# Kernel tuning notes

Hardware: AMD Instinct MI355X
Metric: run time of the kernel (lower is better)

The kernel has to match this reference:

```python
import jax, jax.numpy as jnp
import numpy as np

B, T, C = 4, 2048, 1024
H = 16
HD = C // H  # 64


def setup_inputs() -> dict:
    key = jax.random.key(0)
    k1, k2, k3 = jax.random.split(key, 3)
    x = jax.random.normal(k1, (B, T, C), dtype=jnp.float32)
    W_attn = jax.random.normal(k2, (C, 3 * C), dtype=jnp.float32) * (1.0 / np.sqrt(C))
    b_attn = jnp.zeros((3 * C,), dtype=jnp.float32)
    W_proj = jax.random.normal(k3, (C, C), dtype=jnp.float32) * (1.0 / np.sqrt(C))
    b_proj = jnp.zeros((C,), dtype=jnp.float32)
    return {"x": x, "W_attn": W_attn, "b_attn": b_attn, "W_proj": W_proj, "b_proj": b_proj}


def reference(x, W_attn, b_attn, W_proj, b_proj):
    Bx, Tx, Cx = x.shape
    qkv = x @ W_attn + b_attn                      # [B,T,3C]
    q, k, v = jnp.split(qkv, 3, axis=-1)
    # [B,T,C] -> [B,H,T,HD]
    q = q.reshape(Bx, Tx, H, HD).transpose(0, 2, 1, 3)
    k = k.reshape(Bx, Tx, H, HD).transpose(0, 2, 1, 3)
    v = v.reshape(Bx, Tx, H, HD).transpose(0, 2, 1, 3)
    att = jnp.einsum('bhqd,bhkd->bhqk', q, k) / jnp.sqrt(jnp.float32(HD))
    causal = jnp.tril(jnp.ones((Tx, Tx), dtype=bool))
    att = jnp.where(causal[None, None], att, -jnp.inf)
    att = jax.nn.softmax(att, axis=-1)
    y = jnp.einsum('bhqk,bhkd->bhqd', att, v)      # [B,H,T,HD]
    y = y.transpose(0, 2, 1, 3).reshape(Bx, Tx, Cx)
    return y @ W_proj + b_proj
```

## Files before the change

### kernel.cpp

```cpp
#include <hip/hip_runtime.h>
#include <hip/hip_bf16.h>

typedef unsigned short u16;
typedef __attribute__((ext_vector_type(8))) short bf16x8;
typedef __attribute__((ext_vector_type(4))) float f32x4;

#define MFMA16(a, b, c) __builtin_amdgcn_mfma_f32_16x16x32_bf16((a), (b), (c), 0, 0, 0)

__device__ __forceinline__ u16 f2bf(float f) {
  union { float f; unsigned u; } v; v.f = f;
  unsigned r = v.u + 0x7fffu + ((v.u >> 16) & 1u);
  return (u16)(r >> 16);
}

__device__ __forceinline__ unsigned pk_trunc(float hi, float lo) {
  union { float f; unsigned u; } a, b; a.f = hi; b.f = lo;
  return __builtin_amdgcn_perm(a.u, b.u, 0x07060302u);
}

__device__ __forceinline__ void gload_lds16(const u16* g, u16* l) {
  __builtin_amdgcn_global_load_lds((const __attribute__((address_space(1))) void*)g,
                                   (__attribute__((address_space(3))) void*)l, 16, 0, 0);
}

__global__ __launch_bounds__(256) void convert_bf16_k(const float* __restrict__ in,
                                                      u16* __restrict__ out, int n) {
  int i = (blockIdx.x * 256 + threadIdx.x) * 8;
  if (i >= n) return;
  float4 v0 = *(const float4*)(in + i);
  float4 v1 = *(const float4*)(in + i + 4);
  uint4 o;
  o.x = (unsigned)f2bf(v0.x) | ((unsigned)f2bf(v0.y) << 16);
  o.y = (unsigned)f2bf(v0.z) | ((unsigned)f2bf(v0.w) << 16);
  o.z = (unsigned)f2bf(v1.x) | ((unsigned)f2bf(v1.y) << 16);
  o.w = (unsigned)f2bf(v1.z) | ((unsigned)f2bf(v1.w) << 16);
  *(uint4*)(out + i) = o;
}

__global__ __launch_bounds__(256) void transpose2_k(const float* __restrict__ Wa, u16* __restrict__ WaT,
                                                    const float* __restrict__ Wp, u16* __restrict__ WpT) {
  __shared__ float tile[64][65];
  int b = blockIdx.x;
  const float* W; u16* Wt; int N, n0, k0;
  if (b < 768) { W = Wa; Wt = WaT; N = 3072; n0 = (b % 48) * 64; k0 = (b / 48) * 64; }
  else { int c = b - 768; W = Wp; Wt = WpT; N = 1024; n0 = (c & 15) * 64; k0 = (c >> 4) * 64; }
  const int tx = threadIdx.x & 63, ty = threadIdx.x >> 6;
#pragma unroll
  for (int i = 0; i < 16; ++i)
    tile[ty + 4 * i][tx] = W[(size_t)(k0 + ty + 4 * i) * N + n0 + tx];
  __syncthreads();
#pragma unroll
  for (int i = 0; i < 16; ++i)
    Wt[(size_t)(n0 + ty + 4 * i) * 1024 + k0 + tx] = f2bf(tile[tx][ty + 4 * i]);
}

#define GEMM_PROLOG                                                                \
  __shared__ u16 As[128 * 32];                                                     \
  __shared__ u16 Bs[128 * 32];                                                     \
  const int tid = threadIdx.x;                                                     \
  const int w = tid >> 6, lane = tid & 63;                                         \
  const int wm = w & 1, wn = w >> 1;                                               \
  const int fr = lane & 15, fg = lane >> 4;                                        \
  const int srow = lane >> 2, skof = (lane & 3) * 8;                               \
  u16* lA = As + w * 1024;                                                         \
  u16* lB = Bs + w * 1024;                                                         \
  f32x4 acc[4][4];                                                                 \
  _Pragma("unroll") for (int i = 0; i < 4; i++)                                    \
      _Pragma("unroll") for (int j = 0; j < 4; j++) acc[i][j] = (f32x4){0, 0, 0, 0};

#define GEMM_KLOOP(Aptr, Btptr, SWAP)                                              \
  {                                                                                \
    const u16* gA0 = (Aptr) + (size_t)(m0 + w * 32 + srow) * 1024 + skof;          \
    const u16* gB0 = (Btptr) + (size_t)(n0 + w * 32 + srow) * 1024 + skof;         \
    for (int kt = 0; kt < 32; ++kt) {                                              \
      const int ko = kt * 32;                                                      \
      gload_lds16(gA0 + ko, lA);                                                   \
      gload_lds16(gA0 + ko + 16 * 1024, lA + 512);                                 \
      gload_lds16(gB0 + ko, lB);                                                   \
      gload_lds16(gB0 + ko + 16 * 1024, lB + 512);                                 \
      __syncthreads();                                                             \
      bf16x8 af[4], bfr[4];                                                        \
      _Pragma("unroll") for (int mb = 0; mb < 4; ++mb)                             \
          af[mb] = *(const bf16x8*)&As[(wm * 64 + mb * 16 + fr) * 32 + fg * 8];    \
      _Pragma("unroll") for (int nb = 0; nb < 4; ++nb)                             \
          bfr[nb] = *(const bf16x8*)&Bs[(wn * 64 + nb * 16 + fr) * 32 + fg * 8];   \
      _Pragma("unroll") for (int mb = 0; mb < 4; ++mb)                             \
          _Pragma("unroll") for (int nb = 0; nb < 4; ++nb)                         \
              acc[mb][nb] = (SWAP) ? MFMA16(bfr[nb], af[mb], acc[mb][nb])          \
                                   : MFMA16(af[mb], bfr[nb], acc[mb][nb]);         \
      __syncthreads();                                                             \
    }                                                                              \
  }

__global__ __launch_bounds__(256) void gemm_qkv(const u16* __restrict__ A,
                                                const u16* __restrict__ Bt,
                                                const float* __restrict__ bias,
                                                u16* __restrict__ Qo, u16* __restrict__ Ko,
                                                u16* __restrict__ Vt) {
  const int m0 = blockIdx.y * 128, n0 = blockIdx.x * 128;
  GEMM_PROLOG
  GEMM_KLOOP(A, Bt, 0)
  const int which = n0 >> 10;
#pragma unroll
  for (int nb = 0; nb < 4; ++nb) {
    const int n = n0 + wn * 64 + nb * 16 + fr;
    const float bs = bias[n];
    const int c = n & 1023, h = c >> 6, hd = c & 63;
#pragma unroll
    for (int mb = 0; mb < 4; ++mb) {
      const int mbase = m0 + wm * 64 + mb * 16 + fg * 4;
      const int bb = mbase >> 11;
      const int t = mbase & 2047;
      if (which == 0) {
        u16* dst = Qo + ((size_t)(bb * 16 + h) * 2048 + t) * 64 + hd;
#pragma unroll
        for (int r = 0; r < 4; ++r) dst[(size_t)r * 64] = f2bf((acc[mb][nb][r] + bs) * 0.125f);
      } else if (which == 1) {
        u16* dst = Ko + ((size_t)(bb * 16 + h) * 2048 + t) * 64 + hd;
#pragma unroll
        for (int r = 0; r < 4; ++r) dst[(size_t)r * 64] = f2bf(acc[mb][nb][r] + bs);
      } else {
        ushort4 pv;
        pv.x = f2bf(acc[mb][nb][0] + bs);
        pv.y = f2bf(acc[mb][nb][1] + bs);
        pv.z = f2bf(acc[mb][nb][2] + bs);
        pv.w = f2bf(acc[mb][nb][3] + bs);
        *(ushort4*)(Vt + ((size_t)(bb * 16 + h) * 64 + hd) * 2048 + t) = pv;
      }
    }
  }
}

__global__ __launch_bounds__(256) void gemm_proj(const u16* __restrict__ A,
                                                 const u16* __restrict__ Bt,
                                                 const float* __restrict__ bias,
                                                 float* __restrict__ O) {
  const int id = blockIdx.x;
  const int m0 = (id >> 3) * 128, n0 = (id & 7) * 128;
  GEMM_PROLOG
  GEMM_KLOOP(A, Bt, 1)
#pragma unroll
  for (int mb = 0; mb < 4; ++mb) {
    const int tg = m0 + wm * 64 + mb * 16 + fr;
#pragma unroll
    for (int nb = 0; nb < 4; ++nb) {
      const int n = n0 + wn * 64 + nb * 16 + 4 * fg;
      const float4 b4 = *(const float4*)(bias + n);
      float4 o;
      o.x = acc[mb][nb][0] + b4.x;
      o.y = acc[mb][nb][1] + b4.y;
      o.z = acc[mb][nb][2] + b4.z;
      o.w = acc[mb][nb][3] + b4.w;
      *(float4*)(O + (size_t)tg * 1024 + n) = o;
    }
  }
}

#define PSTR 72
__global__ __launch_bounds__(256) void attn_k(const u16* __restrict__ Q,
                                              const u16* __restrict__ Kb,
                                              const u16* __restrict__ Vt,
                                              u16* __restrict__ Y) {
  __shared__ u16 Ks[64 * 72];
  __shared__ u16 Vs[64 * 72];
  __shared__ u16 Ps[4 * 32 * PSTR];
  const int L = blockIdx.x;
  const int xcd = L & 7, slot = L >> 3;
  const int bh = xcd * 8 + (slot & 7);
  const int qt = 15 - (slot >> 3);
  const int tid = threadIdx.x, w = tid >> 6, lane = tid & 63;
  const int fr = lane & 15, fg = lane >> 4;
  const u16* Qp = Q + (size_t)bh * 2048 * 64;
  const u16* Kp = Kb + (size_t)bh * 2048 * 64;
  const u16* Vp = Vt + (size_t)bh * 64 * 2048;
  const int qw = qt * 128 + w * 32;

  bf16x8 qa[2][2];
#pragma unroll
  for (int g = 0; g < 2; ++g)
#pragma unroll
    for (int c = 0; c < 2; ++c)
      qa[g][c] = *(const bf16x8*)(Qp + (size_t)(qw + g * 16 + fr) * 64 + c * 32 + fg * 8);

  float li[2] = {0.f, 0.f};
  f32x4 ot[2][4];
#pragma unroll
  for (int g = 0; g < 2; ++g)
#pragma unroll
    for (int mb = 0; mb < 4; ++mb) ot[g][mb] = (f32x4){0, 0, 0, 0};

  const int srow = tid >> 2, scol = (tid & 3) * 16;
  u16* Pw = Ps + w * 32 * PSTR;
  const int nk = 2 * qt + 2;
  const u16* Kg = Kp + (size_t)srow * 64 + scol;
  const u16* Vg = Vp + (size_t)srow * 2048 + scol;

  uint4 kr0 = *(const uint4*)(Kg);
  uint4 kr1 = *(const uint4*)(Kg + 8);
  uint4 vr0 = *(const uint4*)(Vg);
  uint4 vr1 = *(const uint4*)(Vg + 8);

  for (int jt = 0; jt < nk; ++jt) {
    const int k0 = jt * 64;
    if (jt) __syncthreads();
    *(uint4*)&Ks[srow * 72 + scol] = kr0;
    *(uint4*)&Ks[srow * 72 + scol + 8] = kr1;
    *(uint4*)&Vs[srow * 72 + scol] = vr0;
    *(uint4*)&Vs[srow * 72 + scol + 8] = vr1;
    __syncthreads();
    if (jt + 1 < nk) {
      const int kn = (jt + 1) * 64;
      kr0 = *(const uint4*)(Kg + (size_t)kn * 64);
      kr1 = *(const uint4*)(Kg + (size_t)kn * 64 + 8);
      vr0 = *(const uint4*)(Vg + kn);
      vr1 = *(const uint4*)(Vg + kn + 8);
    }
    if (k0 > qw + 31) continue;

    bf16x8 kb[4][2];
#pragma unroll
    for (int nb = 0; nb < 4; ++nb) {
      kb[nb][0] = *(const bf16x8*)&Ks[(nb * 16 + fr) * 72 + fg * 8];
      kb[nb][1] = *(const bf16x8*)&Ks[(nb * 16 + fr) * 72 + 32 + fg * 8];
    }
    f32x4 st[2][4];
#pragma unroll
    for (int g = 0; g < 2; ++g)
#pragma unroll
      for (int nb = 0; nb < 4; ++nb) {
        f32x4 z = (f32x4){0, 0, 0, 0};
        z = MFMA16(kb[nb][0], qa[g][0], z);
        z = MFMA16(kb[nb][1], qa[g][1], z);
        st[g][nb] = z;
      }
    const bool needmask = (k0 + 63 > qw);
#pragma unroll
    for (int g = 0; g < 2; ++g) {
      const int q = qw + g * 16 + fr;
      float rs0 = 0.f, rs1 = 0.f;
#pragma unroll
      for (int nb = 0; nb < 4; ++nb) {
        const int kcb = k0 + nb * 16 + 4 * fg;
        float p0 = __expf(st[g][nb][0]);
        float p1 = __expf(st[g][nb][1]);
        float p2 = __expf(st[g][nb][2]);
        float p3 = __expf(st[g][nb][3]);
        if (needmask) {
          p0 = (kcb + 0 > q) ? 0.f : p0;
          p1 = (kcb + 1 > q) ? 0.f : p1;
          p2 = (kcb + 2 > q) ? 0.f : p2;
          p3 = (kcb + 3 > q) ? 0.f : p3;
        }
        rs0 += p0 + p1;
        rs1 += p2 + p3;
        *(uint2*)&Pw[(g * 16 + fr) * PSTR + nb * 16 + 4 * fg] =
            make_uint2(pk_trunc(p1, p0), pk_trunc(p3, p2));
      }
      li[g] += rs0 + rs1;
    }
    bf16x8 pa[2][2];
#pragma unroll
    for (int g = 0; g < 2; ++g)
#pragma unroll
      for (int H = 0; H < 2; ++H)
        pa[g][H] = *(const bf16x8*)&Pw[(g * 16 + fr) * PSTR + H * 32 + fg * 8];
#pragma unroll
    for (int mb = 0; mb < 4; ++mb) {
      bf16x8 vb0 = *(const bf16x8*)&Vs[(mb * 16 + fr) * 72 + fg * 8];
      bf16x8 vb1 = *(const bf16x8*)&Vs[(mb * 16 + fr) * 72 + 32 + fg * 8];
#pragma unroll
      for (int g = 0; g < 2; ++g) {
        ot[g][mb] = MFMA16(vb0, pa[g][0], ot[g][mb]);
        ot[g][mb] = MFMA16(vb1, pa[g][1], ot[g][mb]);
      }
    }
  }

  const int b = bh >> 4, h = bh & 15;
#pragma unroll
  for (int g = 0; g < 2; ++g) {
    float l = li[g];
    l += __shfl_xor(l, 16);
    l += __shfl_xor(l, 32);
    const float inv = 1.0f / l;
    const int t = qw + g * 16 + fr;
    u16* yrow = Y + ((size_t)b * 2048 + t) * 1024 + h * 64;
#pragma unroll
    for (int mb = 0; mb < 4; ++mb) {
      const unsigned d0 = (unsigned)f2bf(ot[g][mb][0] * inv) |
                          ((unsigned)f2bf(ot[g][mb][1] * inv) << 16);
      const unsigned d1 = (unsigned)f2bf(ot[g][mb][2] * inv) |
                          ((unsigned)f2bf(ot[g][mb][3] * inv) << 16);
      *(uint2*)&yrow[mb * 16 + fg * 4] = make_uint2(d0, d1);
    }
  }
}

extern "C" void kernel_launch(void* const* d_in, const int* in_sizes, int n_in,
                              void* d_out, int out_size, void* d_ws, size_t ws_size,
                              hipStream_t stream) {
  const float* x = (const float*)d_in[0];
  const float* Wa = (const float*)d_in[1];
  const float* ba = (const float*)d_in[2];
  const float* Wp = (const float*)d_in[3];
  const float* bp = (const float*)d_in[4];
  float* out = (float*)d_out;

  char* p = (char*)d_ws;
  u16* xb = (u16*)p;   p += (size_t)8192 * 1024 * 2;
  u16* WaT = (u16*)p;  p += (size_t)3072 * 1024 * 2;
  u16* WpT = (u16*)p;  p += (size_t)1024 * 1024 * 2;
  u16* Qb = (u16*)p;   p += (size_t)64 * 2048 * 64 * 2;
  u16* Kbuf = (u16*)p; p += (size_t)64 * 2048 * 64 * 2;
  u16* Vtb = (u16*)p;  p += (size_t)64 * 64 * 2048 * 2;
  u16* Yb = (u16*)p;   p += (size_t)8192 * 1024 * 2;

  convert_bf16_k<<<4096, 256, 0, stream>>>(x, xb, 8192 * 1024);
  transpose2_k<<<1024, 256, 0, stream>>>(Wa, WaT, Wp, WpT);
  gemm_qkv<<<dim3(24, 64), 256, 0, stream>>>(xb, WaT, ba, Qb, Kbuf, Vtb);
  attn_k<<<1024, 256, 0, stream>>>(Qb, Kbuf, Vtb, Yb);
  gemm_proj<<<512, 256, 0, stream>>>(Yb, WpT, bp, out);
}
```

Measured before the change: 269.3 us.

## Rewrite QKV GEMM as 256x256 tile, 8-wave, double-buffered pipelined kernel

Replaces the 128x128 single-buffered QKV GEMM with a 256x256-tile kernel of 512 threads. Each block double-buffers K=64 slices in LDS and interleaves global-to-LDS loads for the next stage between four MFMA phases, using explicit barriers, waitcnt and setprio. It also swizzles the LDS layout and remaps block indices for L2 locality. The goal is to hide global load latency and raise MFMA utilization, at the cost of more LDS and register use and fragile hand-written synchronization.

```diff
diff --git a/kernel.cpp b/kernel.cpp
--- a/kernel.cpp
+++ b/kernel.cpp
@@ -92,14 +92,92 @@
     }                                                                              \
   }
 
-__global__ __launch_bounds__(256) void gemm_qkv(const u16* __restrict__ A,
-                                                const u16* __restrict__ Bt,
-                                                const float* __restrict__ bias,
-                                                u16* __restrict__ Qo, u16* __restrict__ Ko,
-                                                u16* __restrict__ Vt) {
-  const int m0 = blockIdx.y * 128, n0 = blockIdx.x * 128;
-  GEMM_PROLOG
-  GEMM_KLOOP(A, Bt, 0)
+#define BAR() asm volatile("s_barrier" ::: "memory")
+#define WLG()                                                   \
+  do {                                                          \
+    asm volatile("s_waitcnt lgkmcnt(0)" ::: "memory");          \
+    __builtin_amdgcn_sched_barrier(0);                          \
+  } while (0)
+
+__global__ __launch_bounds__(512, 2) void gemm_qkv_8p(const u16* __restrict__ A,
+                                                      const u16* __restrict__ Bt,
+                                                      const float* __restrict__ bias,
+                                                      u16* __restrict__ Qo, u16* __restrict__ Ko,
+                                                      u16* __restrict__ Vt) {
+  __shared__ u16 sm[2][2][16384];
+  const int bid = blockIdx.x;
+  const int swz = (bid & 7) * 48 + (bid >> 3);
+  const int m0 = (swz / 12) * 256, n0 = (swz % 12) * 256;
+  const int tid = threadIdx.x, w = tid >> 6, lane = tid & 63;
+  const int wm = w >> 2, wn = w & 3;
+  const int fr = lane & 15, fg = lane >> 4;
+
+  const int sr = lane >> 2;
+  const int sk = (lane & 1) * 8 + ((((lane >> 1) ^ (lane >> 5)) & 1) << 4);
+  const int kc = (w & 1) * 32 + sk;
+  const int r0 = (w >> 1) * 16 + sr;
+  const int lsw = fr * 32 + ((fg * 8) ^ ((fr & 8) ? 16 : 0));
+
+  const u16* gA00 = A + (size_t)(m0 + r0) * 1024 + kc;
+  const u16* gB00 = Bt + (size_t)(n0 + r0) * 1024 + kc;
+
+#define STG_(mat, base, tt, h, c)                                                    \
+  gload_lds16((base) + (size_t)(h) * 131072 + (c) * 65536 + (size_t)(tt) * 64,       \
+              &sm[(tt) & 1][mat][(h) * 8192 + (c) * 4096 + w * 512])
+
+  f32x4 acc[8][4];
+#pragma unroll
+  for (int i = 0; i < 8; ++i)
+#pragma unroll
+    for (int j = 0; j < 4; ++j) acc[i][j] = (f32x4){0, 0, 0, 0};
+
+  STG_(0, gA00, 0, 0, 0); STG_(0, gA00, 0, 0, 1);
+  STG_(0, gA00, 0, 1, 0); STG_(0, gA00, 0, 1, 1);
+  STG_(1, gB00, 0, 0, 0); STG_(1, gB00, 0, 0, 1);
+  STG_(1, gB00, 0, 1, 0); STG_(1, gB00, 0, 1, 1);
+  STG_(1, gB00, 1, 0, 0); STG_(1, gB00, 1, 0, 1);
+  asm volatile("s_waitcnt vmcnt(2)" ::: "memory");
+  BAR();
+
+#define LDA4(KK, MB0)                                                     \
+  _Pragma("unroll") for (int i = 0; i < 4; ++i)                           \
+      av[i] = *(const bf16x8*)(ard + ((MB0 + i) * 2 + (KK)) * 512);
+#define LDB4(KK)                                                          \
+  _Pragma("unroll") for (int i = 0; i < 4; ++i)                           \
+      bv[i] = *(const bf16x8*)(brd + (i * 2 + (KK)) * 512);
+#define MM16(MB0)                                                         \
+  __builtin_amdgcn_s_setprio(1);                                          \
+  _Pragma("unroll") for (int i = 0; i < 4; ++i)                           \
+      _Pragma("unroll") for (int j = 0; j < 4; ++j)                       \
+          acc[MB0 + i][j] = MFMA16(av[i], bv[j], acc[MB0 + i][j]);        \
+  __builtin_amdgcn_s_setprio(0);
+
+  for (int t = 0; t < 16; ++t) {
+    const int b = t & 1;
+    const u16* ard = &sm[b][0][wm * 8192 + lsw];
+    const u16* brd = &sm[b][1][(wn >> 1) * 8192 + (wn & 1) * 4096 + lsw];
+    bf16x8 av[4], bv[4];
+
+    LDA4(0, 0); LDB4(0);
+    if (t + 1 < 16) { STG_(1, gB00, t + 1, 1, 0); STG_(1, gB00, t + 1, 1, 1); }
+    BAR(); WLG(); MM16(0); BAR();
+
+    LDA4(0, 4);
+    if (t + 1 < 16) { STG_(0, gA00, t + 1, 0, 0); STG_(0, gA00, t + 1, 0, 1); }
+    BAR(); WLG(); MM16(4); BAR();
+
+    LDA4(1, 0); LDB4(1);
+    if (t + 1 < 16) { STG_(0, gA00, t + 1, 1, 0); STG_(0, gA00, t + 1, 1, 1); }
+    BAR(); WLG(); MM16(0); BAR();
+
+    LDA4(1, 4);
+    if (t + 2 < 16) { STG_(1, gB00, t + 2, 0, 0); STG_(1, gB00, t + 2, 0, 1); }
+    BAR(); WLG(); MM16(4);
+    if (t + 2 < 16)      asm volatile("s_waitcnt vmcnt(2)" ::: "memory");
+    else if (t + 1 < 16) asm volatile("s_waitcnt vmcnt(0)" ::: "memory");
+    BAR();
+  }
+
   const int which = n0 >> 10;
 #pragma unroll
   for (int nb = 0; nb < 4; ++nb) {
@@ -107,16 +185,16 @@
     const float bs = bias[n];
     const int c = n & 1023, h = c >> 6, hd = c & 63;
 #pragma unroll
-    for (int mb = 0; mb < 4; ++mb) {
-      const int mbase = m0 + wm * 64 + mb * 16 + fg * 4;
+    for (int mb = 0; mb < 8; ++mb) {
+      const int mbase = m0 + wm * 128 + mb * 16 + fg * 4;
       const int bb = mbase >> 11;
-      const int t = mbase & 2047;
+      const int tt = mbase & 2047;
       if (which == 0) {
-        u16* dst = Qo + ((size_t)(bb * 16 + h) * 2048 + t) * 64 + hd;
+        u16* dst = Qo + ((size_t)(bb * 16 + h) * 2048 + tt) * 64 + hd;
 #pragma unroll
         for (int r = 0; r < 4; ++r) dst[(size_t)r * 64] = f2bf((acc[mb][nb][r] + bs) * 0.125f);
       } else if (which == 1) {
-        u16* dst = Ko + ((size_t)(bb * 16 + h) * 2048 + t) * 64 + hd;
+        u16* dst = Ko + ((size_t)(bb * 16 + h) * 2048 + tt) * 64 + hd;
 #pragma unroll
         for (int r = 0; r < 4; ++r) dst[(size_t)r * 64] = f2bf(acc[mb][nb][r] + bs);
       } else {
@@ -125,7 +203,7 @@
         pv.y = f2bf(acc[mb][nb][1] + bs);
         pv.z = f2bf(acc[mb][nb][2] + bs);
         pv.w = f2bf(acc[mb][nb][3] + bs);
-        *(ushort4*)(Vt + ((size_t)(bb * 16 + h) * 64 + hd) * 2048 + t) = pv;
+        *(ushort4*)(Vt + ((size_t)(bb * 16 + h) * 64 + hd) * 2048 + tt) = pv;
       }
     }
   }
@@ -317,7 +395,7 @@
 
   convert_bf16_k<<<4096, 256, 0, stream>>>(x, xb, 8192 * 1024);
   transpose2_k<<<1024, 256, 0, stream>>>(Wa, WaT, Wp, WpT);
-  gemm_qkv<<<dim3(24, 64), 256, 0, stream>>>(xb, WaT, ba, Qb, Kbuf, Vtb);
+  gemm_qkv_8p<<<384, 512, 0, stream>>>(xb, WaT, ba, Qb, Kbuf, Vtb);
   attn_k<<<1024, 256, 0, stream>>>(Qb, Kbuf, Vtb, Yb);
   gemm_proj<<<512, 256, 0, stream>>>(Yb, WpT, bp, out);
 }
```

Result: faster. 262.6 us (-2.5%).

## Rewrite QKV and projection GEMMs as double-buffered 8-wave 256-tile kernels

Applied to the files above, without the earlier changes.

Both GEMMs move from 128x128 tiles with 4 waves and a single LDS buffer to 512-thread blocks with 256-wide tiles (256x256 for QKV, 256x128 for proj) and a K-step of 64. Each step prefetches the next tile into a second LDS buffer while MFMAs run on the current one. The kernels also add XOR-swizzled LDS addressing, XCD-aware block swizzling, s_setprio around the MFMA bursts, and explicit waitcnt/barrier scheduling. The aim is to hide global-load latency and raise data reuse per block, at the cost of more LDS and registers per block and a proj epilogue that now uses scalar strided stores.

```diff
diff --git a/kernel.cpp b/kernel.cpp
--- a/kernel.cpp
+++ b/kernel.cpp
@@ -54,52 +54,97 @@
     Wt[(size_t)(n0 + ty + 4 * i) * 1024 + k0 + tx] = f2bf(tile[tx][ty + 4 * i]);
 }
 
-#define GEMM_PROLOG                                                                \
-  __shared__ u16 As[128 * 32];                                                     \
-  __shared__ u16 Bs[128 * 32];                                                     \
-  const int tid = threadIdx.x;                                                     \
-  const int w = tid >> 6, lane = tid & 63;                                         \
-  const int wm = w & 1, wn = w >> 1;                                               \
-  const int fr = lane & 15, fg = lane >> 4;                                        \
-  const int srow = lane >> 2, skof = (lane & 3) * 8;                               \
-  u16* lA = As + w * 1024;                                                         \
-  u16* lB = Bs + w * 1024;                                                         \
-  f32x4 acc[4][4];                                                                 \
-  _Pragma("unroll") for (int i = 0; i < 4; i++)                                    \
-      _Pragma("unroll") for (int j = 0; j < 4; j++) acc[i][j] = (f32x4){0, 0, 0, 0};
-
-#define GEMM_KLOOP(Aptr, Btptr, SWAP)                                              \
-  {                                                                                \
-    const u16* gA0 = (Aptr) + (size_t)(m0 + w * 32 + srow) * 1024 + skof;          \
-    const u16* gB0 = (Btptr) + (size_t)(n0 + w * 32 + srow) * 1024 + skof;         \
-    for (int kt = 0; kt < 32; ++kt) {                                              \
-      const int ko = kt * 32;                                                      \
-      gload_lds16(gA0 + ko, lA);                                                   \
-      gload_lds16(gA0 + ko + 16 * 1024, lA + 512);                                 \
-      gload_lds16(gB0 + ko, lB);                                                   \
-      gload_lds16(gB0 + ko + 16 * 1024, lB + 512);                                 \
-      __syncthreads();                                                             \
-      bf16x8 af[4], bfr[4];                                                        \
-      _Pragma("unroll") for (int mb = 0; mb < 4; ++mb)                             \
-          af[mb] = *(const bf16x8*)&As[(wm * 64 + mb * 16 + fr) * 32 + fg * 8];    \
-      _Pragma("unroll") for (int nb = 0; nb < 4; ++nb)                             \
-          bfr[nb] = *(const bf16x8*)&Bs[(wn * 64 + nb * 16 + fr) * 32 + fg * 8];   \
-      _Pragma("unroll") for (int mb = 0; mb < 4; ++mb)                             \
-          _Pragma("unroll") for (int nb = 0; nb < 4; ++nb)                         \
-              acc[mb][nb] = (SWAP) ? MFMA16(bfr[nb], af[mb], acc[mb][nb])          \
-                                   : MFMA16(af[mb], bfr[nb], acc[mb][nb]);         \
-      __syncthreads();                                                             \
-    }                                                                              \
-  }
-
-__global__ __launch_bounds__(256) void gemm_qkv(const u16* __restrict__ A,
-                                                const u16* __restrict__ Bt,
-                                                const float* __restrict__ bias,
-                                                u16* __restrict__ Qo, u16* __restrict__ Ko,
-                                                u16* __restrict__ Vt) {
-  const int m0 = blockIdx.y * 128, n0 = blockIdx.x * 128;
-  GEMM_PROLOG
-  GEMM_KLOOP(A, Bt, 0)
+#define BAR() asm volatile("s_barrier" ::: "memory")
+#define WLG()                                                   \
+  do {                                                          \
+    asm volatile("s_waitcnt lgkmcnt(0)" ::: "memory");          \
+    __builtin_amdgcn_sched_barrier(0);                          \
+  } while (0)
+#define VMW0() asm volatile("s_waitcnt vmcnt(0)" ::: "memory")
+
+#define LANE_CONSTS                                                       \
+  const int tid = threadIdx.x, w = tid >> 6, lane = tid & 63;             \
+  const int wm = w >> 2, wn = w & 3;                                      \
+  const int fr = lane & 15, fg = lane >> 4;                               \
+  const int sr = lane >> 2;                                               \
+  const int sk = (lane & 1) * 8 + ((((lane >> 1) ^ (lane >> 5)) & 1) << 4); \
+  const int kc = (w & 1) * 32 + sk;                                       \
+  const int r0g = (w >> 1) * 16 + sr;                                     \
+  const int lsw = fr * 32 + ((fg * 8) ^ ((fr & 8) ? 16 : 0));
+
+__global__ __launch_bounds__(512, 2) void gemm_qkv_8p(const u16* __restrict__ A,
+                                                      const u16* __restrict__ Bt,
+                                                      const float* __restrict__ bias,
+                                                      u16* __restrict__ Qo, u16* __restrict__ Ko,
+                                                      u16* __restrict__ Vt) {
+  __shared__ u16 sm[2][32768];
+  const int bid = blockIdx.x;
+  const int swz = (bid & 7) * 48 + (bid >> 3);
+  const int m0 = (swz / 12) * 256, n0 = (swz % 12) * 256;
+  LANE_CONSTS
+  const int aoff = wm * 8192 + lsw;
+  const int boff = 16384 + (wn >> 1) * 8192 + (wn & 1) * 4096 + lsw;
+
+  const u16* gA = A + (size_t)(m0 + r0g) * 1024 + kc;
+  const u16* gB = Bt + (size_t)(n0 + r0g) * 1024 + kc;
+
+#define QSTGA(D, H, C) \
+  gload_lds16(gA + (size_t)(H) * 131072 + (C) * 65536, &sm[(D)][(H) * 8192 + (C) * 4096 + w * 512])
+#define QSTGB(D, H, C) \
+  gload_lds16(gB + (size_t)(H) * 131072 + (C) * 65536, &sm[(D)][16384 + (H) * 8192 + (C) * 4096 + w * 512])
+
+  f32x4 acc[8][4];
+#pragma unroll
+  for (int i = 0; i < 8; ++i)
+#pragma unroll
+    for (int j = 0; j < 4; ++j) acc[i][j] = (f32x4){0, 0, 0, 0};
+
+  QSTGA(0, 0, 0); QSTGA(0, 0, 1); QSTGA(0, 1, 0); QSTGA(0, 1, 1);
+  QSTGB(0, 0, 0); QSTGB(0, 0, 1); QSTGB(0, 1, 0); QSTGB(0, 1, 1);
+  gA += 64; gB += 64;
+  VMW0(); BAR();
+
+#define QLDA(B_, KK, M0_)                                                 \
+  _Pragma("unroll") for (int i = 0; i < 4; ++i)                           \
+      av[i] = *(const bf16x8*)&sm[(B_)][aoff + (((M0_) + i) * 2 + (KK)) * 512];
+#define QLDB(B_, KK)                                                      \
+  _Pragma("unroll") for (int i = 0; i < 4; ++i)                           \
+      bv[i] = *(const bf16x8*)&sm[(B_)][boff + (i * 2 + (KK)) * 512];
+#define QMM(MB0)                                                          \
+  __builtin_amdgcn_s_setprio(1);                                          \
+  _Pragma("unroll") for (int i = 0; i < 4; ++i)                           \
+      _Pragma("unroll") for (int j = 0; j < 4; ++j)                       \
+          acc[(MB0) + i][j] = MFMA16(av[i], bv[j], acc[(MB0) + i][j]);    \
+  __builtin_amdgcn_s_setprio(0);
+
+#define QTILE(B_, S_)                                                          \
+  {                                                                            \
+    bf16x8 av[4], bv[4];                                                       \
+                       \
+    QLDA(B_, 0, 0) QLDB(B_, 0)                                                 \
+    if (S_) { QSTGA((B_) ^ 1, 0, 0); QSTGA((B_) ^ 1, 0, 1);                    \
+              QSTGA((B_) ^ 1, 1, 0); QSTGA((B_) ^ 1, 1, 1); }                  \
+    BAR(); WLG(); QMM(0) BAR();                                                \
+                               \
+    QLDA(B_, 0, 4)                                                             \
+    if (S_) { QSTGB((B_) ^ 1, 0, 0); QSTGB((B_) ^ 1, 0, 1);                    \
+              QSTGB((B_) ^ 1, 1, 0); QSTGB((B_) ^ 1, 1, 1); }                  \
+    BAR(); WLG(); QMM(4) BAR();                                                \
+                                                  \
+    QLDA(B_, 1, 0) QLDB(B_, 1)                                                 \
+    BAR(); WLG(); QMM(0) BAR();                                                \
+                       \
+    QLDA(B_, 1, 4)                                                             \
+    BAR(); WLG(); QMM(4)                                                       \
+    if (S_) { VMW0(); gA += 64; gB += 64; }                                    \
+    BAR();                                                                     \
+  }
+
+#pragma unroll 1
+  for (int tp = 0; tp < 7; ++tp) { QTILE(0, 1) QTILE(1, 1) }
+  QTILE(0, 1)
+  QTILE(1, 0)
+
   const int which = n0 >> 10;
 #pragma unroll
   for (int nb = 0; nb < 4; ++nb) {
@@ -107,16 +152,16 @@
     const float bs = bias[n];
     const int c = n & 1023, h = c >> 6, hd = c & 63;
 #pragma unroll
-    for (int mb = 0; mb < 4; ++mb) {
-      const int mbase = m0 + wm * 64 + mb * 16 + fg * 4;
+    for (int mb = 0; mb < 8; ++mb) {
+      const int mbase = m0 + wm * 128 + mb * 16 + fg * 4;
       const int bb = mbase >> 11;
-      const int t = mbase & 2047;
+      const int tt = mbase & 2047;
       if (which == 0) {
-        u16* dst = Qo + ((size_t)(bb * 16 + h) * 2048 + t) * 64 + hd;
+        u16* dst = Qo + ((size_t)(bb * 16 + h) * 2048 + tt) * 64 + hd;
 #pragma unroll
         for (int r = 0; r < 4; ++r) dst[(size_t)r * 64] = f2bf((acc[mb][nb][r] + bs) * 0.125f);
       } else if (which == 1) {
-        u16* dst = Ko + ((size_t)(bb * 16 + h) * 2048 + t) * 64 + hd;
+        u16* dst = Ko + ((size_t)(bb * 16 + h) * 2048 + tt) * 64 + hd;
 #pragma unroll
         for (int r = 0; r < 4; ++r) dst[(size_t)r * 64] = f2bf(acc[mb][nb][r] + bs);
       } else {
@@ -125,35 +170,102 @@
         pv.y = f2bf(acc[mb][nb][1] + bs);
         pv.z = f2bf(acc[mb][nb][2] + bs);
         pv.w = f2bf(acc[mb][nb][3] + bs);
-        *(ushort4*)(Vt + ((size_t)(bb * 16 + h) * 64 + hd) * 2048 + t) = pv;
+        *(ushort4*)(Vt + ((size_t)(bb * 16 + h) * 64 + hd) * 2048 + tt) = pv;
       }
     }
   }
-}
-
-__global__ __launch_bounds__(256) void gemm_proj(const u16* __restrict__ A,
-                                                 const u16* __restrict__ Bt,
-                                                 const float* __restrict__ bias,
-                                                 float* __restrict__ O) {
-  const int id = blockIdx.x;
-  const int m0 = (id >> 3) * 128, n0 = (id & 7) * 128;
-  GEMM_PROLOG
-  GEMM_KLOOP(A, Bt, 1)
-#pragma unroll
-  for (int mb = 0; mb < 4; ++mb) {
-    const int tg = m0 + wm * 64 + mb * 16 + fr;
-#pragma unroll
-    for (int nb = 0; nb < 4; ++nb) {
-      const int n = n0 + wn * 64 + nb * 16 + 4 * fg;
-      const float4 b4 = *(const float4*)(bias + n);
-      float4 o;
-      o.x = acc[mb][nb][0] + b4.x;
-      o.y = acc[mb][nb][1] + b4.y;
-      o.z = acc[mb][nb][2] + b4.z;
-      o.w = acc[mb][nb][3] + b4.w;
-      *(float4*)(O + (size_t)tg * 1024 + n) = o;
-    }
-  }
+#undef QSTGA
+#undef QSTGB
+#undef QLDA
+#undef QLDB
+#undef QMM
+#undef QTILE
+}
+
+__global__ __launch_bounds__(512, 2) void gemm_proj_8p(const u16* __restrict__ A,
+                                                       const u16* __restrict__ Bt,
+                                                       const float* __restrict__ bias,
+                                                       float* __restrict__ O) {
+  __shared__ u16 sm[2][24576];
+  const int bid = blockIdx.x;
+  const int swz = (bid & 7) * 32 + (bid >> 3);
+  const int m0 = (swz >> 3) * 256, n0 = (swz & 7) * 128;
+  LANE_CONSTS
+  const int aoff = wm * 8192 + lsw;
+  const int boff = 16384 + wn * 2048 + lsw;
+
+  const u16* gA = A + (size_t)(m0 + r0g) * 1024 + kc;
+  const u16* gB = Bt + (size_t)(n0 + r0g) * 1024 + kc;
+
+#define PSTGA(D, H, C) \
+  gload_lds16(gA + (size_t)(H) * 131072 + (C) * 65536, &sm[(D)][(H) * 8192 + (C) * 4096 + w * 512])
+#define PSTGB(D, C) \
+  gload_lds16(gB + (size_t)(C) * 65536, &sm[(D)][16384 + (C) * 4096 + w * 512])
+
+  f32x4 acc[8][2];
+#pragma unroll
+  for (int i = 0; i < 8; ++i)
+#pragma unroll
+    for (int j = 0; j < 2; ++j) acc[i][j] = (f32x4){0, 0, 0, 0};
+
+  PSTGA(0, 0, 0); PSTGA(0, 0, 1); PSTGA(0, 1, 0); PSTGA(0, 1, 1);
+  PSTGB(0, 0); PSTGB(0, 1);
+  gA += 64; gB += 64;
+  VMW0(); BAR();
+
+#define PLDA(B_, KK, M0_)                                                 \
+  _Pragma("unroll") for (int i = 0; i < 4; ++i)                           \
+      av[i] = *(const bf16x8*)&sm[(B_)][aoff + (((M0_) + i) * 2 + (KK)) * 512];
+#define PLDB(B_, KK)                                                      \
+  _Pragma("unroll") for (int i = 0; i < 2; ++i)                           \
+      bv[i] = *(const bf16x8*)&sm[(B_)][boff + (i * 2 + (KK)) * 512];
+#define PMM(MB0)                                                          \
+  __builtin_amdgcn_s_setprio(1);                                          \
+  _Pragma("unroll") for (int i = 0; i < 4; ++i)                           \
+      _Pragma("unroll") for (int j = 0; j < 2; ++j)                       \
+          acc[(MB0) + i][j] = MFMA16(av[i], bv[j], acc[(MB0) + i][j]);    \
+  __builtin_amdgcn_s_setprio(0);
+
+#define PTILE(B_, S_)                                                          \
+  {                                                                            \
+    bf16x8 av[4], bv[2];                                                       \
+    PLDA(B_, 0, 0) PLDB(B_, 0)                                                 \
+    if (S_) { PSTGA((B_) ^ 1, 0, 0); PSTGA((B_) ^ 1, 0, 1);                    \
+              PSTGA((B_) ^ 1, 1, 0); PSTGA((B_) ^ 1, 1, 1); }                  \
+    BAR(); WLG(); PMM(0) BAR();                                                \
+    PLDA(B_, 0, 4)                                                             \
+    if (S_) { PSTGB((B_) ^ 1, 0); PSTGB((B_) ^ 1, 1); }                        \
+    BAR(); WLG(); PMM(4) BAR();                                                \
+    PLDA(B_, 1, 0) PLDB(B_, 1)                                                 \
+    BAR(); WLG(); PMM(0) BAR();                                                \
+    PLDA(B_, 1, 4)                                                             \
+    BAR(); WLG(); PMM(4)                                                       \
+    if (S_) { VMW0(); gA += 64; gB += 64; }                                    \
+    BAR();                                                                     \
+  }
+
+#pragma unroll 1
+  for (int tp = 0; tp < 7; ++tp) { PTILE(0, 1) PTILE(1, 1) }
+  PTILE(0, 1)
+  PTILE(1, 0)
+
+#pragma unroll
+  for (int nb = 0; nb < 2; ++nb) {
+    const int n = n0 + wn * 32 + nb * 16 + fr;
+    const float bs = bias[n];
+#pragma unroll
+    for (int mb = 0; mb < 8; ++mb) {
+      const int tg = m0 + wm * 128 + mb * 16 + fg * 4;
+#pragma unroll
+      for (int r = 0; r < 4; ++r) O[(size_t)(tg + r) * 1024 + n] = acc[mb][nb][r] + bs;
+    }
+  }
+#undef PSTGA
+#undef PSTGB
+#undef PLDA
+#undef PLDB
+#undef PMM
+#undef PTILE
 }
 
 #define PSTR 72
@@ -317,7 +429,7 @@
 
   convert_bf16_k<<<4096, 256, 0, stream>>>(x, xb, 8192 * 1024);
   transpose2_k<<<1024, 256, 0, stream>>>(Wa, WaT, Wp, WpT);
-  gemm_qkv<<<dim3(24, 64), 256, 0, stream>>>(xb, WaT, ba, Qb, Kbuf, Vtb);
+  gemm_qkv_8p<<<384, 512, 0, stream>>>(xb, WaT, ba, Qb, Kbuf, Vtb);
   attn_k<<<1024, 256, 0, stream>>>(Qb, Kbuf, Vtb, Yb);
-  gemm_proj<<<512, 256, 0, stream>>>(Yb, WpT, bp, out);
-}
+  gemm_proj_8p<<<256, 512, 0, stream>>>(Yb, WpT, bp, out);
+}
```

After: 254.3 us. -5.6%, faster.

## Double-buffer GEMM K-loop with swizzled LDS, larger QKV tiles, XCD-aware block mapping

Applied to the files above, without the earlier changes.

Both projection GEMMs are rewritten to double-buffer LDS so the next K-slice's global-to-LDS loads are issued before the current slice's MFMAs, which halves the barriers per K step. LDS columns are XOR-swizzled to reduce bank conflicts. The QKV GEMM moves to 128x256 tiles with each wave owning a 128x64 slab, and block IDs are remapped so consecutive blocks land on the same XCD for L2 reuse. The projection GEMM's epilogue now writes scalars in a different pattern, and the larger accumulator tiles raise register pressure.

```diff
diff --git a/kernel.cpp b/kernel.cpp
--- a/kernel.cpp
+++ b/kernel.cpp
@@ -54,69 +54,89 @@
     Wt[(size_t)(n0 + ty + 4 * i) * 1024 + k0 + tx] = f2bf(tile[tx][ty + 4 * i]);
 }
 
-#define GEMM_PROLOG                                                                \
-  __shared__ u16 As[128 * 32];                                                     \
-  __shared__ u16 Bs[128 * 32];                                                     \
-  const int tid = threadIdx.x;                                                     \
-  const int w = tid >> 6, lane = tid & 63;                                         \
-  const int wm = w & 1, wn = w >> 1;                                               \
-  const int fr = lane & 15, fg = lane >> 4;                                        \
-  const int srow = lane >> 2, skof = (lane & 3) * 8;                               \
-  u16* lA = As + w * 1024;                                                         \
-  u16* lB = Bs + w * 1024;                                                         \
-  f32x4 acc[4][4];                                                                 \
-  _Pragma("unroll") for (int i = 0; i < 4; i++)                                    \
-      _Pragma("unroll") for (int j = 0; j < 4; j++) acc[i][j] = (f32x4){0, 0, 0, 0};
-
-#define GEMM_KLOOP(Aptr, Btptr, SWAP)                                              \
-  {                                                                                \
-    const u16* gA0 = (Aptr) + (size_t)(m0 + w * 32 + srow) * 1024 + skof;          \
-    const u16* gB0 = (Btptr) + (size_t)(n0 + w * 32 + srow) * 1024 + skof;         \
-    for (int kt = 0; kt < 32; ++kt) {                                              \
-      const int ko = kt * 32;                                                      \
-      gload_lds16(gA0 + ko, lA);                                                   \
-      gload_lds16(gA0 + ko + 16 * 1024, lA + 512);                                 \
-      gload_lds16(gB0 + ko, lB);                                                   \
-      gload_lds16(gB0 + ko + 16 * 1024, lB + 512);                                 \
-      __syncthreads();                                                             \
-      bf16x8 af[4], bfr[4];                                                        \
-      _Pragma("unroll") for (int mb = 0; mb < 4; ++mb)                             \
-          af[mb] = *(const bf16x8*)&As[(wm * 64 + mb * 16 + fr) * 32 + fg * 8];    \
-      _Pragma("unroll") for (int nb = 0; nb < 4; ++nb)                             \
-          bfr[nb] = *(const bf16x8*)&Bs[(wn * 64 + nb * 16 + fr) * 32 + fg * 8];   \
-      _Pragma("unroll") for (int mb = 0; mb < 4; ++mb)                             \
-          _Pragma("unroll") for (int nb = 0; nb < 4; ++nb)                         \
-              acc[mb][nb] = (SWAP) ? MFMA16(bfr[nb], af[mb], acc[mb][nb])          \
-                                   : MFMA16(af[mb], bfr[nb], acc[mb][nb]);         \
-      __syncthreads();                                                             \
-    }                                                                              \
-  }
-
-__global__ __launch_bounds__(256) void gemm_qkv(const u16* __restrict__ A,
-                                                const u16* __restrict__ Bt,
-                                                const float* __restrict__ bias,
-                                                u16* __restrict__ Qo, u16* __restrict__ Ko,
-                                                u16* __restrict__ Vt) {
-  const int m0 = blockIdx.y * 128, n0 = blockIdx.x * 128;
-  GEMM_PROLOG
-  GEMM_KLOOP(A, Bt, 0)
+
+#define GEMM_LANE_CONSTS                                                    \
+  const int tid = threadIdx.x, w = tid >> 6, lane = tid & 63;               \
+  const int fr = lane & 15, fg = lane >> 4;                                 \
+  const int swS = ((fr >> 1) & 3) << 3;                                     \
+  const int srow = tid >> 2;                                                \
+  const int scol = ((tid & 3) * 8) ^ (((tid >> 3) & 3) << 3);
+
+__global__ __launch_bounds__(256, 2) void gemm_qkv_v2(const u16* __restrict__ A,
+                                                      const u16* __restrict__ Bt,
+                                                      const float* __restrict__ bias,
+                                                      u16* __restrict__ Qo, u16* __restrict__ Ko,
+                                                      u16* __restrict__ Vt) {
+  __shared__ u16 sm[2][12288];
+  const int bid = blockIdx.x;
+  const int swz = (bid & 7) * 96 + (bid >> 3);
+  const int m0 = (swz / 12) * 128, n0 = (swz % 12) * 256;
+  GEMM_LANE_CONSTS
+
+  const u16* gA = A + (size_t)(m0 + srow) * 1024 + scol;
+  const u16* gB = Bt + (size_t)(n0 + srow) * 1024 + scol;
+
+#define VSTGA(D, C) gload_lds16(gA + (size_t)(C) * 65536, &sm[(D)][(C) * 2048 + tid * 8])
+#define VSTGB(D, C) gload_lds16(gB + (size_t)(C) * 65536, &sm[(D)][4096 + (C) * 2048 + tid * 8])
+
+  f32x4 acc[8][4];
+#pragma unroll
+  for (int i = 0; i < 8; ++i)
+#pragma unroll
+    for (int j = 0; j < 4; ++j) acc[i][j] = (f32x4){0, 0, 0, 0};
+
+  VSTGA(0, 0); VSTGA(0, 1);
+  VSTGB(0, 0); VSTGB(0, 1); VSTGB(0, 2); VSTGB(0, 3);
+  gA += 32; gB += 32;
+  __syncthreads();
+
+  const int aoff = fr * 32 + ((fg * 8) ^ swS);
+  const int boff = 4096 + w * 2048 + fr * 32 + ((fg * 8) ^ swS);
+
+#define VTILE(B_, S_)                                                          \
+  {                                                                            \
+    if (S_) { VSTGA((B_) ^ 1, 0); VSTGA((B_) ^ 1, 1);                          \
+              VSTGB((B_) ^ 1, 0); VSTGB((B_) ^ 1, 1);                          \
+              VSTGB((B_) ^ 1, 2); VSTGB((B_) ^ 1, 3); }                        \
+    bf16x8 av[4], bv[4];                                                       \
+    _Pragma("unroll") for (int nb = 0; nb < 4; ++nb)                           \
+        bv[nb] = *(const bf16x8*)&sm[(B_)][boff + nb * 512];                   \
+    _Pragma("unroll") for (int i = 0; i < 4; ++i)                              \
+        av[i] = *(const bf16x8*)&sm[(B_)][aoff + i * 512];                     \
+    _Pragma("unroll") for (int i = 0; i < 4; ++i)                              \
+        _Pragma("unroll") for (int nb = 0; nb < 4; ++nb)                       \
+            acc[i][nb] = MFMA16(av[i], bv[nb], acc[i][nb]);                    \
+    _Pragma("unroll") for (int i = 0; i < 4; ++i)                              \
+        av[i] = *(const bf16x8*)&sm[(B_)][aoff + (4 + i) * 512];               \
+    _Pragma("unroll") for (int i = 0; i < 4; ++i)                              \
+        _Pragma("unroll") for (int nb = 0; nb < 4; ++nb)                       \
+            acc[4 + i][nb] = MFMA16(av[i], bv[nb], acc[4 + i][nb]);            \
+    if (S_) { gA += 32; gB += 32; }                                            \
+    __syncthreads();                                                           \
+  }
+
+#pragma unroll 1
+  for (int tp = 0; tp < 15; ++tp) { VTILE(0, 1) VTILE(1, 1) }
+  VTILE(0, 1)
+  VTILE(1, 0)
+
   const int which = n0 >> 10;
 #pragma unroll
   for (int nb = 0; nb < 4; ++nb) {
-    const int n = n0 + wn * 64 + nb * 16 + fr;
+    const int n = n0 + w * 64 + nb * 16 + fr;
     const float bs = bias[n];
     const int c = n & 1023, h = c >> 6, hd = c & 63;
 #pragma unroll
-    for (int mb = 0; mb < 4; ++mb) {
-      const int mbase = m0 + wm * 64 + mb * 16 + fg * 4;
+    for (int mb = 0; mb < 8; ++mb) {
+      const int mbase = m0 + mb * 16 + fg * 4;
       const int bb = mbase >> 11;
-      const int t = mbase & 2047;
+      const int tt = mbase & 2047;
       if (which == 0) {
-        u16* dst = Qo + ((size_t)(bb * 16 + h) * 2048 + t) * 64 + hd;
+        u16* dst = Qo + ((size_t)(bb * 16 + h) * 2048 + tt) * 64 + hd;
 #pragma unroll
         for (int r = 0; r < 4; ++r) dst[(size_t)r * 64] = f2bf((acc[mb][nb][r] + bs) * 0.125f);
       } else if (which == 1) {
-        u16* dst = Ko + ((size_t)(bb * 16 + h) * 2048 + t) * 64 + hd;
+        u16* dst = Ko + ((size_t)(bb * 16 + h) * 2048 + tt) * 64 + hd;
 #pragma unroll
         for (int r = 0; r < 4; ++r) dst[(size_t)r * 64] = f2bf(acc[mb][nb][r] + bs);
       } else {
@@ -125,35 +145,85 @@
         pv.y = f2bf(acc[mb][nb][1] + bs);
         pv.z = f2bf(acc[mb][nb][2] + bs);
         pv.w = f2bf(acc[mb][nb][3] + bs);
-        *(ushort4*)(Vt + ((size_t)(bb * 16 + h) * 64 + hd) * 2048 + t) = pv;
+        *(ushort4*)(Vt + ((size_t)(bb * 16 + h) * 64 + hd) * 2048 + tt) = pv;
       }
     }
   }
-}
-
-__global__ __launch_bounds__(256) void gemm_proj(const u16* __restrict__ A,
-                                                 const u16* __restrict__ Bt,
-                                                 const float* __restrict__ bias,
-                                                 float* __restrict__ O) {
-  const int id = blockIdx.x;
-  const int m0 = (id >> 3) * 128, n0 = (id & 7) * 128;
-  GEMM_PROLOG
-  GEMM_KLOOP(A, Bt, 1)
-#pragma unroll
-  for (int mb = 0; mb < 4; ++mb) {
-    const int tg = m0 + wm * 64 + mb * 16 + fr;
-#pragma unroll
-    for (int nb = 0; nb < 4; ++nb) {
-      const int n = n0 + wn * 64 + nb * 16 + 4 * fg;
-      const float4 b4 = *(const float4*)(bias + n);
-      float4 o;
-      o.x = acc[mb][nb][0] + b4.x;
-      o.y = acc[mb][nb][1] + b4.y;
-      o.z = acc[mb][nb][2] + b4.z;
-      o.w = acc[mb][nb][3] + b4.w;
-      *(float4*)(O + (size_t)tg * 1024 + n) = o;
-    }
-  }
+#undef VSTGA
+#undef VSTGB
+#undef VTILE
+}
+
+__global__ __launch_bounds__(256, 4) void gemm_proj_v2(const u16* __restrict__ A,
+                                                       const u16* __restrict__ Bt,
+                                                       const float* __restrict__ bias,
+                                                       float* __restrict__ O) {
+  __shared__ u16 sm[2][8192];
+  const int bid = blockIdx.x;
+  const int swz = (bid & 7) * 64 + (bid >> 3);
+  const int m0 = (swz >> 3) * 128, n0 = (swz & 7) * 128;
+  GEMM_LANE_CONSTS
+
+  const u16* gA = A + (size_t)(m0 + srow) * 1024 + scol;
+  const u16* gB = Bt + (size_t)(n0 + srow) * 1024 + scol;
+
+#define PSTGA(D, C) gload_lds16(gA + (size_t)(C) * 65536, &sm[(D)][(C) * 2048 + tid * 8])
+#define PSTGB(D, C) gload_lds16(gB + (size_t)(C) * 65536, &sm[(D)][4096 + (C) * 2048 + tid * 8])
+
+  f32x4 acc[8][2];
+#pragma unroll
+  for (int i = 0; i < 8; ++i)
+#pragma unroll
+    for (int j = 0; j < 2; ++j) acc[i][j] = (f32x4){0, 0, 0, 0};
+
+  PSTGA(0, 0); PSTGA(0, 1);
+  PSTGB(0, 0); PSTGB(0, 1);
+  gA += 32; gB += 32;
+  __syncthreads();
+
+  const int aoff = fr * 32 + ((fg * 8) ^ swS);
+  const int boff = 4096 + w * 1024 + fr * 32 + ((fg * 8) ^ swS);
+
+#define PTILE(B_, S_)                                                          \
+  {                                                                            \
+    if (S_) { PSTGA((B_) ^ 1, 0); PSTGA((B_) ^ 1, 1);                          \
+              PSTGB((B_) ^ 1, 0); PSTGB((B_) ^ 1, 1); }                        \
+    bf16x8 av[4], bv[2];                                                       \
+    _Pragma("unroll") for (int nb = 0; nb < 2; ++nb)                           \
+        bv[nb] = *(const bf16x8*)&sm[(B_)][boff + nb * 512];                   \
+    _Pragma("unroll") for (int i = 0; i < 4; ++i)                              \
+        av[i] = *(const bf16x8*)&sm[(B_)][aoff + i * 512];                     \
+    _Pragma("unroll") for (int i = 0; i < 4; ++i)                              \
+        _Pragma("unroll") for (int nb = 0; nb < 2; ++nb)                       \
+            acc[i][nb] = MFMA16(av[i], bv[nb], acc[i][nb]);                    \
+    _Pragma("unroll") for (int i = 0; i < 4; ++i)                              \
+        av[i] = *(const bf16x8*)&sm[(B_)][aoff + (4 + i) * 512];               \
+    _Pragma("unroll") for (int i = 0; i < 4; ++i)                              \
+        _Pragma("unroll") for (int nb = 0; nb < 2; ++nb)                       \
+            acc[4 + i][nb] = MFMA16(av[i], bv[nb], acc[4 + i][nb]);            \
+    if (S_) { gA += 32; gB += 32; }                                            \
+    __syncthreads();                                                           \
+  }
+
+#pragma unroll 1
+  for (int tp = 0; tp < 15; ++tp) { PTILE(0, 1) PTILE(1, 1) }
+  PTILE(0, 1)
+  PTILE(1, 0)
+
+#pragma unroll
+  for (int nb = 0; nb < 2; ++nb) {
+    const int n = n0 + w * 32 + nb * 16 + fr;
+    const float bs = bias[n];
+#pragma unroll
+    for (int mb = 0; mb < 8; ++mb) {
+      const int tg = m0 + mb * 16 + fg * 4;
+#pragma unroll
+      for (int r = 0; r < 4; ++r) O[(size_t)(tg + r) * 1024 + n] = acc[mb][nb][r] + bs;
+    }
+  }
+#undef PSTGA
+#undef PSTGB
+#undef PTILE
 }
 
 #define PSTR 72
@@ -317,7 +387,7 @@
 
   convert_bf16_k<<<4096, 256, 0, stream>>>(x, xb, 8192 * 1024);
   transpose2_k<<<1024, 256, 0, stream>>>(Wa, WaT, Wp, WpT);
-  gemm_qkv<<<dim3(24, 64), 256, 0, stream>>>(xb, WaT, ba, Qb, Kbuf, Vtb);
+  gemm_qkv_v2<<<768, 256, 0, stream>>>(xb, WaT, ba, Qb, Kbuf, Vtb);
   attn_k<<<1024, 256, 0, stream>>>(Qb, Kbuf, Vtb, Yb);
-  gemm_proj<<<512, 256, 0, stream>>>(Yb, WpT, bp, out);
-}
+  gemm_proj_v2<<<512, 256, 0, stream>>>(Yb, WpT, bp, out);
+}
```

After: 250.6 us. 1.07x faster.
